# Kernel optimization log

Hardware: AMD Instinct MI355X
Metric: run time of the kernel (lower is better)

## Reference

```python
import jax, jax.numpy as jnp
import numpy as np

M, N, D, L, DEPTH, WIDTH, BATCH = 64, 4096, 64, 32, 4, 256, 1024
WIN = 2 * L + 1


def setup_inputs() -> dict:
    key = jax.random.key(0)
    ks = jax.random.split(key, 5)
    u = jax.random.normal(ks[0], (BATCH, D), dtype=jnp.float32)
    # xavier-style scaled gaussians for weights, zeros for biases (matches torch init pattern)
    weight0 = jax.random.normal(ks[1], (M, WIDTH, D), dtype=jnp.float32) * (2.0 / (WIDTH + D)) ** 0.5
    bias0 = jnp.zeros((M, WIDTH, 1), dtype=jnp.float32)
    weight = jax.random.normal(ks[2], (DEPTH - 1, M, WIDTH, WIDTH), dtype=jnp.float32) * (1.0 / WIDTH) ** 0.5
    bias = jnp.zeros((DEPTH - 1, M, WIDTH, 1), dtype=jnp.float32)
    weight_final = jax.random.normal(ks[3], (M, WIN, WIDTH), dtype=jnp.float32) * (2.0 / (WIN + WIDTH)) ** 0.5
    bias_final = jnp.zeros((M, WIN, 1), dtype=jnp.float32)
    xi = jax.random.normal(ks[4], (M, N + 2 * L), dtype=jnp.float32) * (2.0 / (M + N + 2 * L)) ** 0.5
    return {"u": u, "weight0": weight0, "bias0": bias0, "weight": weight,
            "bias": bias, "weight_final": weight_final, "bias_final": bias_final, "xi": xi}


def reference(u, weight0, bias0, weight, bias, weight_final, bias_final, xi) -> jnp.ndarray:
    act = jax.nn.sigmoid
    # per-M shared MLP: u1 [M, width, batch]
    u1 = act(jnp.einsum('mwd,bd->mwb', weight0, u) + bias0)
    for i in range(weight.shape[0]):  # small fixed depth loop
        u1 = act(jnp.einsum('mwv,mvb->mwb', weight[i], u1) + bias[i])
    G = act(jnp.einsum('mjw,mwb->mjb', weight_final, u1) + bias_final)
    # sliding-window correlation: out[n, b] = sum_{m,j} xi[m, n+j] * G[m, j, b]
    win = G.shape[1]
    n_out = xi.shape[1] - (win - 1)
    idx = jnp.arange(n_out)[:, None] + jnp.arange(win)[None, :]
    xw = xi[:, idx]
    return jnp.einsum('mnj,mjb->nb', xw, G)  # [N, batch]
```

## Files before the change

kernel.cpp:

```cpp
#include <hip/hip_runtime.h>
#include <math.h>

typedef __attribute__((ext_vector_type(8))) short short8;
typedef __attribute__((ext_vector_type(4))) float floatx4;
typedef __attribute__((ext_vector_type(4))) unsigned short ushort4v;

__device__ __forceinline__ void load_lds16(const void* g, void* l) {
    __builtin_amdgcn_global_load_lds((const __attribute__((address_space(1))) void*)g,
                                     (__attribute__((address_space(3))) void*)l,
                                     16, 0, 0);
}

__device__ __forceinline__ unsigned short f2bf(float x) {
    union { float f; unsigned int u; } v; v.f = x;
    unsigned int r = v.u + 0x7fffu + ((v.u >> 16) & 1u);
    return (unsigned short)(r >> 16);
}

__device__ __forceinline__ float sigm(float x) { return 1.0f / (1.0f + __expf(-x)); }

__global__ void prep(const float* __restrict__ w0, const float* __restrict__ w,
                     const float* __restrict__ wf, const float* __restrict__ xi,
                     unsigned short* __restrict__ w0d, unsigned short* __restrict__ wd,
                     unsigned short* __restrict__ wfd, unsigned int* __restrict__ xw) {
    const int bid = blockIdx.x;
    if (bid < 1024) {
        int i = bid * 256 + threadIdx.x;
        float4 v = ((const float4*)w0)[i];
        ((ushort4v*)w0d)[i] = (ushort4v){ f2bf(v.x), f2bf(v.y), f2bf(v.z), f2bf(v.w) };
    } else if (bid < 13312) {
        int i = (bid - 1024) * 256 + threadIdx.x;
        float4 v = ((const float4*)w)[i];
        ((ushort4v*)wd)[i] = (ushort4v){ f2bf(v.x), f2bf(v.y), f2bf(v.z), f2bf(v.w) };
    } else if (bid < 15360) {
        int idx = (bid - 13312) * 256 + threadIdx.x;
        int e = idx * 4;
        int m = e >> 15, r = (e >> 8) & 127, c = e & 255;
        ushort4v o = {0, 0, 0, 0};
        if (r < 65) {
            float4 v = *(const float4*)&wf[((size_t)m * 65 + r) * 256 + c];
            o = (ushort4v){ f2bf(v.x), f2bf(v.y), f2bf(v.z), f2bf(v.w) };
        }
        ((ushort4v*)wfd)[idx] = o;
    } else {
        const int n = bid - 15360;
        #pragma unroll
        for (int t = 0; t < 9; ++t) {
            const int idx = t * 256 + threadIdx.x;
            if (idx < 2176) {
                const int m = idx / 34;
                const int pos = idx - m * 34;
                const int j0 = pos * 2;
                const float* xim = xi + (size_t)m * 4160 + n;
                const float v0 = (j0 < 65) ? xim[j0] : 0.0f;
                const float v1 = (j0 + 1 < 65) ? xim[j0 + 1] : 0.0f;
                xw[(size_t)n * 2176 + idx] =
                    (unsigned int)f2bf(v0) | ((unsigned int)f2bf(v1) << 16);
            }
        }
    }
}

template<int K, int I>
__device__ __forceinline__ void mlp_mfma(
    const unsigned short* __restrict__ Wm, const unsigned short* src,
    int wave, int lane, floatx4 (*acc)[4])
{
    const int quad = lane >> 4, l16 = lane & 15;
    const int rbw = wave * (I * 16);
    const floatx4 zero = {0.f, 0.f, 0.f, 0.f};
    #pragma unroll
    for (int i = 0; i < I; ++i)
        #pragma unroll
        for (int j = 0; j < 4; ++j) acc[i][j] = zero;

    short8 af[I];
    #pragma unroll
    for (int i = 0; i < I; ++i)
        af[i] = *(const short8*)&Wm[(size_t)(rbw + i * 16 + l16) * K + quad * 8];

    #pragma unroll
    for (int kk = 0; kk < K / 32; ++kk) {
        short8 afn[I];
        if (kk + 1 < K / 32) {
            #pragma unroll
            for (int i = 0; i < I; ++i)
                afn[i] = *(const short8*)&Wm[(size_t)(rbw + i * 16 + l16) * K + (kk + 1) * 32 + quad * 8];
        }
        short8 bf[4];
        #pragma unroll
        for (int j = 0; j < 4; ++j) {
            const int cb = j * 16 + l16;
            bf[j] = *(const short8*)&src[cb * K + (((kk * 4 + quad) ^ (cb & 7)) * 8)];
        }
        #pragma unroll
        for (int i = 0; i < I; ++i)
            #pragma unroll
            for (int j = 0; j < 4; ++j)
                acc[i][j] = __builtin_amdgcn_mfma_f32_16x16x32_bf16(af[i], bf[j], acc[i][j], 0, 0, 0);
        #pragma unroll
        for (int i = 0; i < I; ++i) af[i] = afn[i];
    }
}

__device__ __forceinline__ void mlp_write(
    const float* __restrict__ bm, unsigned short* dst,
    int wave, int lane, floatx4 (*acc)[4])
{
    const int quad = lane >> 4, l16 = lane & 15;
    const int rbw = wave * 64;
    #pragma unroll
    for (int i = 0; i < 4; ++i) {
        const int rb = rbw + i * 16 + quad * 4;
        float bv0 = bm[rb], bv1 = bm[rb + 1], bv2 = bm[rb + 2], bv3 = bm[rb + 3];
        #pragma unroll
        for (int j = 0; j < 4; ++j) {
            const int cb = j * 16 + l16;
            ushort4v o;
            o[0] = f2bf(sigm(acc[i][j][0] + bv0));
            o[1] = f2bf(sigm(acc[i][j][1] + bv1));
            o[2] = f2bf(sigm(acc[i][j][2] + bv2));
            o[3] = f2bf(sigm(acc[i][j][3] + bv3));
            *(ushort4v*)&dst[cb * 256 + (((rb >> 3) ^ (cb & 7)) * 8) + (rb & 7)] = o;
        }
    }
}

__global__ __launch_bounds__(256, 2)
void fused_mlp(const float* __restrict__ u,
               const unsigned short* __restrict__ w0_bf, const float* __restrict__ b0_,
               const unsigned short* __restrict__ w_bf,  const float* __restrict__ b_,
               const unsigned short* __restrict__ wf_bf, const float* __restrict__ bf_,
               unsigned short* __restrict__ Gflat) {
    __shared__ unsigned short X[64 * 256];

    const int bid = blockIdx.x;
    const int xcd = bid & 7, slot = bid >> 3;
    const int m  = (xcd << 3) + (slot >> 4);
    const int b0 = (slot & 15) << 6;
    const int tid = threadIdx.x, wave = tid >> 6, lane = tid & 63;

    {
        const int b = tid >> 2, dc = tid & 3;
        const float* up = u + (size_t)(b0 + b) * 64 + dc * 16;
        float4 v0 = *(const float4*)(up);
        float4 v1 = *(const float4*)(up + 4);
        float4 v2 = *(const float4*)(up + 8);
        float4 v3 = *(const float4*)(up + 12);
        short8 c0 = { (short)f2bf(v0.x), (short)f2bf(v0.y), (short)f2bf(v0.z), (short)f2bf(v0.w),
                      (short)f2bf(v1.x), (short)f2bf(v1.y), (short)f2bf(v1.z), (short)f2bf(v1.w) };
        short8 c1 = { (short)f2bf(v2.x), (short)f2bf(v2.y), (short)f2bf(v2.z), (short)f2bf(v2.w),
                      (short)f2bf(v3.x), (short)f2bf(v3.y), (short)f2bf(v3.z), (short)f2bf(v3.w) };
        *(short8*)&X[b * 64 + (((dc * 2)     ^ (b & 7)) * 8)] = c0;
        *(short8*)&X[b * 64 + (((dc * 2 + 1) ^ (b & 7)) * 8)] = c1;
    }
    __syncthreads();

    floatx4 acc[4][4];

    mlp_mfma<64, 4>(w0_bf + (size_t)m * 16384, X, wave, lane, acc);
    __syncthreads();
    mlp_write(b0_ + (size_t)m * 256, X, wave, lane, acc);
    __syncthreads();

    #pragma unroll 1
    for (int l = 0; l < 3; ++l) {
        mlp_mfma<256, 4>(w_bf + ((size_t)l * 64 + m) * 65536, X, wave, lane, acc);
        __syncthreads();
        mlp_write(b_ + ((size_t)l * 64 + m) * 256, X, wave, lane, acc);
        __syncthreads();
    }

    {
        floatx4 acf[2][4];
        mlp_mfma<256, 2>(wf_bf + (size_t)m * 32768, X, wave, lane, acf);
        const int quad = lane >> 4, l16 = lane & 15;
        const float* bm = bf_ + (size_t)m * 65;
        unsigned short* Gg = Gflat + (size_t)b0 * 4352 + m * 68;
        #pragma unroll
        for (int i = 0; i < 2; ++i) {
            const int rb = wave * 32 + i * 16 + quad * 4;
            if (rb < 68) {
                float bv[4];
                #pragma unroll
                for (int rr = 0; rr < 4; ++rr)
                    bv[rr] = (rb + rr < 65) ? bm[rb + rr] : 0.0f;
                #pragma unroll
                for (int j = 0; j < 4; ++j) {
                    const int cb = j * 16 + l16;
                    ushort4v o;
                    #pragma unroll
                    for (int rr = 0; rr < 4; ++rr)
                        o[rr] = f2bf(sigm(acf[i][j][rr] + bv[rr]));
                    *(ushort4v*)&Gg[(size_t)cb * 4352 + rb] = o;
                }
            }
        }
    }
}

__global__ __launch_bounds__(256, 3)
void contract_gemm(const unsigned short* __restrict__ XW,
                   const unsigned short* __restrict__ G,
                   float* __restrict__ P) {
    const int bid = blockIdx.x;
    const int xcd = bid & 7, slot = bid >> 3;
    const int kc  = slot >> 5;
    const int rst = slot & 31;
    const int r0 = ((xcd << 2) + (rst >> 3)) << 7;
    const int c0 = (rst & 7) << 7;
    const int kb = kc * 1088;
    float* Pc = P + (size_t)kc * 4096 * 1024;

    __shared__ unsigned short As[128 * 64];
    __shared__ unsigned short Bs[128 * 64];

    const int tid = threadIdx.x;
    const int wave = tid >> 6, lane = tid & 63;
    const int quad = lane >> 4, l16 = lane & 15;
    const int wr = (wave & 1) * 64;
    const int wc = (wave >> 1) * 64;
    const int srow = wave * 32 + (lane >> 3);
    const int spos = lane & 7;

    floatx4 acc[4][4];
    const floatx4 zero = {0.f, 0.f, 0.f, 0.f};
    #pragma unroll
    for (int i = 0; i < 4; ++i)
        #pragma unroll
        for (int j = 0; j < 4; ++j) acc[i][j] = zero;

    for (int k0 = kb; k0 < kb + 1088; k0 += 64) {
        #pragma unroll
        for (int t = 0; t < 4; ++t) {
            const int row = srow + t * 8;
            const int fc  = spos ^ (row & 7);
            load_lds16(XW + (size_t)(r0 + row) * 4352 + k0 + fc * 8,
                       &As[(wave * 32 + t * 8) * 64]);
            load_lds16(G + (size_t)(c0 + row) * 4352 + k0 + fc * 8,
                       &Bs[(wave * 32 + t * 8) * 64]);
        }
        __syncthreads();

        #pragma unroll
        for (int kk = 0; kk < 2; ++kk) {
            short8 af[4], bfr[4];
            #pragma unroll
            for (int i = 0; i < 4; ++i) {
                const int ra = wr + i * 16 + l16;
                af[i]  = *(const short8*)&As[ra * 64 + (((kk * 4 + quad) ^ (ra & 7)) * 8)];
                const int cb = wc + i * 16 + l16;
                bfr[i] = *(const short8*)&Bs[cb * 64 + (((kk * 4 + quad) ^ (cb & 7)) * 8)];
            }
            #pragma unroll
            for (int i = 0; i < 4; ++i)
                #pragma unroll
                for (int j = 0; j < 4; ++j)
                    acc[i][j] = __builtin_amdgcn_mfma_f32_16x16x32_bf16(af[i], bfr[j], acc[i][j], 0, 0, 0);
        }
        __syncthreads();
    }

    #pragma unroll
    for (int i = 0; i < 4; ++i) {
        const int rb = r0 + wr + i * 16 + quad * 4;
        #pragma unroll
        for (int rr = 0; rr < 4; ++rr)
            #pragma unroll
            for (int j = 0; j < 4; ++j) {
                const int col = c0 + wc + j * 16 + l16;
                Pc[(size_t)(rb + rr) * 1024 + col] = acc[i][j][rr];
            }
    }
}

__global__ void reduce4(const float* __restrict__ P, float* __restrict__ out) {
    const int i = blockIdx.x * 256 + threadIdx.x;
    const float4* p = (const float4*)P;
    float4 a = p[i], b = p[i + 1048576], c = p[i + 2097152], d = p[i + 3145728];
    ((float4*)out)[i] = (float4){ a.x + b.x + c.x + d.x, a.y + b.y + c.y + d.y,
                                  a.z + b.z + c.z + d.z, a.w + b.w + c.w + d.w };
}

extern "C" void kernel_launch(void* const* d_in, const int* in_sizes, int n_in,
                              void* d_out, int out_size, void* d_ws, size_t ws_size,
                              hipStream_t stream) {
    const float* u   = (const float*)d_in[0];
    const float* w0  = (const float*)d_in[1];
    const float* b0_ = (const float*)d_in[2];
    const float* w   = (const float*)d_in[3];
    const float* b   = (const float*)d_in[4];
    const float* wf  = (const float*)d_in[5];
    const float* bf_ = (const float*)d_in[6];
    const float* xi  = (const float*)d_in[7];
    float* out = (float*)d_out;

    unsigned short* w0_bf = (unsigned short*)d_ws;
    unsigned short* w_bf  = w0_bf + 1048576;
    unsigned short* wf_bf = w_bf  + 12582912;
    unsigned short* Gflat = wf_bf + 2097152;
    unsigned short* XW    = Gflat + 4456448;
    float*          P     = (float*)(XW + 17825792);

    prep<<<19456, 256, 0, stream>>>(w0, w, wf, xi, w0_bf, w_bf, wf_bf, (unsigned int*)XW);
    fused_mlp<<<1024, 256, 0, stream>>>(u, w0_bf, b0_, w_bf, b, wf_bf, bf_, Gflat);
    contract_gemm<<<1024, 256, 0, stream>>>(XW, Gflat, P);
    reduce4<<<4096, 256, 0, stream>>>(P, out);
}
```

Measured before the change: 263.9 us.

## Pre-tile bf16 weights into MFMA fragment order for coalesced A-operand loads

The prep kernel now writes the bf16 weight copies in a fragment-tiled layout, ordered by row block, k-step and lane, so each lane's 16-byte A fragment sits contiguously with its wave neighbours. The MLP MFMA loop reads these tiles with fully coalesced 1KB-per-wave loads instead of strided row reads. Each prep thread now converts 8 elements instead of 4, so fewer prep blocks are launched. The risk is more complex index math in prep and a dependence on the consumer's exact tile order, including the zero padding of the final weight rows.

```diff
diff --git a/kernel.cpp b/kernel.cpp
--- a/kernel.cpp
+++ b/kernel.cpp
@@ -24,26 +24,48 @@
                      unsigned short* __restrict__ w0d, unsigned short* __restrict__ wd,
                      unsigned short* __restrict__ wfd, unsigned int* __restrict__ xw) {
     const int bid = blockIdx.x;
-    if (bid < 1024) {
-        int i = bid * 256 + threadIdx.x;
-        float4 v = ((const float4*)w0)[i];
-        ((ushort4v*)w0d)[i] = (ushort4v){ f2bf(v.x), f2bf(v.y), f2bf(v.z), f2bf(v.w) };
-    } else if (bid < 13312) {
-        int i = (bid - 1024) * 256 + threadIdx.x;
-        float4 v = ((const float4*)w)[i];
-        ((ushort4v*)wd)[i] = (ushort4v){ f2bf(v.x), f2bf(v.y), f2bf(v.z), f2bf(v.w) };
-    } else if (bid < 15360) {
-        int idx = (bid - 13312) * 256 + threadIdx.x;
-        int e = idx * 4;
-        int m = e >> 15, r = (e >> 8) & 127, c = e & 255;
-        ushort4v o = {0, 0, 0, 0};
+    if (bid < 6656) {
+        const bool is0 = bid < 512;
+        const int c = (is0 ? bid : bid - 512) * 256 + threadIdx.x;
+        const int cpm = is0 ? 2048 : 8192;
+        const int Kk  = is0 ? 2 : 8;
+        const int K   = Kk * 32;
+        const int mm  = c / cpm;
+        const int cm  = c - mm * cpm;
+        const int rblk = cm >> 6 >= 0 ? (cm / (Kk * 64)) : 0;
+        const int rem  = cm - rblk * (Kk * 64);
+        const int kk   = rem >> 6;
+        const int lane = rem & 63;
+        const int r  = rblk * 16 + (lane & 15);
+        const int k0 = kk * 32 + (lane >> 4) * 8;
+        const float* srcp = (is0 ? w0 : w) + ((size_t)mm * 256 + r) * K + k0;
+        unsigned short* dstp = (is0 ? w0d : wd) + (size_t)c * 8;
+        float4 a = *(const float4*)srcp;
+        float4 b = *(const float4*)(srcp + 4);
+        short8 o = { (short)f2bf(a.x), (short)f2bf(a.y), (short)f2bf(a.z), (short)f2bf(a.w),
+                     (short)f2bf(b.x), (short)f2bf(b.y), (short)f2bf(b.z), (short)f2bf(b.w) };
+        *(short8*)dstp = o;
+    } else if (bid < 7680) {
+        const int c = (bid - 6656) * 256 + threadIdx.x;
+        const int m  = c >> 12;
+        const int cm = c & 4095;
+        const int rblk = cm >> 9;
+        const int rem  = cm & 511;
+        const int kk   = rem >> 6;
+        const int lane = rem & 63;
+        const int r  = rblk * 16 + (lane & 15);
+        const int k0 = kk * 32 + (lane >> 4) * 8;
+        short8 o = {0,0,0,0,0,0,0,0};
         if (r < 65) {
-            float4 v = *(const float4*)&wf[((size_t)m * 65 + r) * 256 + c];
-            o = (ushort4v){ f2bf(v.x), f2bf(v.y), f2bf(v.z), f2bf(v.w) };
-        }
-        ((ushort4v*)wfd)[idx] = o;
+            const float* srcp = wf + ((size_t)m * 65 + r) * 256 + k0;
+            float4 a = *(const float4*)srcp;
+            float4 b = *(const float4*)(srcp + 4);
+            o = (short8){ (short)f2bf(a.x), (short)f2bf(a.y), (short)f2bf(a.z), (short)f2bf(a.w),
+                          (short)f2bf(b.x), (short)f2bf(b.y), (short)f2bf(b.z), (short)f2bf(b.w) };
+        }
+        *(short8*)(wfd + (size_t)c * 8) = o;
     } else {
-        const int n = bid - 15360;
+        const int n = bid - 7680;
         #pragma unroll
         for (int t = 0; t < 9; ++t) {
             const int idx = t * 256 + threadIdx.x;
@@ -63,11 +85,12 @@
 
 template<int K, int I>
 __device__ __forceinline__ void mlp_mfma(
-    const unsigned short* __restrict__ Wm, const unsigned short* src,
+    const unsigned short* __restrict__ Wt, const unsigned short* src,
     int wave, int lane, floatx4 (*acc)[4])
 {
+    const int Kk = K / 32;
     const int quad = lane >> 4, l16 = lane & 15;
-    const int rbw = wave * (I * 16);
+    const int rblk0 = wave * I;
     const floatx4 zero = {0.f, 0.f, 0.f, 0.f};
     #pragma unroll
     for (int i = 0; i < I; ++i)
@@ -77,15 +100,15 @@
     short8 af[I];
     #pragma unroll
     for (int i = 0; i < I; ++i)
-        af[i] = *(const short8*)&Wm[(size_t)(rbw + i * 16 + l16) * K + quad * 8];
-
-    #pragma unroll
-    for (int kk = 0; kk < K / 32; ++kk) {
+        af[i] = *(const short8*)&Wt[(size_t)(((rblk0 + i) * Kk + 0) * 64 + lane) * 8];
+
+    #pragma unroll
+    for (int kk = 0; kk < Kk; ++kk) {
         short8 afn[I];
-        if (kk + 1 < K / 32) {
+        if (kk + 1 < Kk) {
             #pragma unroll
             for (int i = 0; i < I; ++i)
-                afn[i] = *(const short8*)&Wm[(size_t)(rbw + i * 16 + l16) * K + (kk + 1) * 32 + quad * 8];
+                afn[i] = *(const short8*)&Wt[(size_t)(((rblk0 + i) * Kk + kk + 1) * 64 + lane) * 8];
         }
         short8 bf[4];
         #pragma unroll
@@ -302,7 +325,7 @@
     unsigned short* XW    = Gflat + 4456448;
     float*          P     = (float*)(XW + 17825792);
 
-    prep<<<19456, 256, 0, stream>>>(w0, w, wf, xi, w0_bf, w_bf, wf_bf, (unsigned int*)XW);
+    prep<<<11776, 256, 0, stream>>>(w0, w, wf, xi, w0_bf, w_bf, wf_bf, (unsigned int*)XW);
     fused_mlp<<<1024, 256, 0, stream>>>(u, w0_bf, b0_, w_bf, b, wf_bf, bf_, Gflat);
     contract_gemm<<<1024, 256, 0, stream>>>(XW, Gflat, P);
     reduce4<<<4096, 256, 0, stream>>>(P, out);
```

Result: no change. 262.6 us (-0.5%).
